# Optimization experiments

Measured on AMD Instinct MI355X. Metric: run time of the kernel, lower is better.

The kernel has to match this reference:

```python
import jax, jax.numpy as jnp
import numpy as np

HIDDEN = 1024
NUM_HEADS = 16
HEAD_SIZE = HIDDEN // NUM_HEADS


def setup_inputs() -> dict:
    key = jax.random.key(0)
    ks = jax.random.split(key, 5)
    B, S = 2, 2048
    x = jax.random.normal(ks[0], (B, S, HIDDEN), dtype=jnp.float32)
    # nn.Linear(hidden, 3*hidden): weight stored (in, out) for x @ W
    scale_qkv = 1.0 / np.sqrt(HIDDEN)
    w_qkv = jax.random.uniform(ks[1], (HIDDEN, 3 * HIDDEN), minval=-scale_qkv, maxval=scale_qkv, dtype=jnp.float32)
    b_qkv = jax.random.uniform(ks[2], (3 * HIDDEN,), minval=-scale_qkv, maxval=scale_qkv, dtype=jnp.float32)
    w_o = jax.random.uniform(ks[3], (HIDDEN, HIDDEN), minval=-scale_qkv, maxval=scale_qkv, dtype=jnp.float32)
    b_o = jax.random.uniform(ks[4], (HIDDEN,), minval=-scale_qkv, maxval=scale_qkv, dtype=jnp.float32)
    return {"x": x, "w_qkv": w_qkv, "b_qkv": b_qkv, "w_o": w_o, "b_o": b_o}


def reference(x, w_qkv, b_qkv, w_o, b_o):
    B, S, H = x.shape
    qkv = x @ w_qkv + b_qkv  # (B, S, 3H)
    q, k, v = jnp.split(qkv, 3, axis=-1)
    # (B, S, H) -> (B, nheads, S, head_size)
    def heads(t):
        return t.reshape(B, S, NUM_HEADS, HEAD_SIZE).transpose(0, 2, 1, 3)
    q, k, v = heads(q), heads(k), heads(v)
    scores = jnp.einsum('bhqd,bhkd->bhqk', q, k) / np.sqrt(HEAD_SIZE).astype(np.float32)
    causal = jnp.tril(jnp.ones((S, S), dtype=bool))  # k <= q
    scores = jnp.where(causal, scores, -jnp.inf)
    probs = jax.nn.softmax(scores, axis=-1)
    out = jnp.einsum('bhqk,bhkd->bqhd', probs, v).reshape(B, S, H)
    return out @ w_o + b_o
```

## Files before the change

kernel.cpp:

```cpp
#include <hip/hip_runtime.h>
#include <stdint.h>


typedef __bf16 bf16;
typedef __attribute__((ext_vector_type(8))) __bf16 bf16x8;
typedef __attribute__((ext_vector_type(4))) __bf16 bf16x4;
typedef __attribute__((ext_vector_type(4))) float floatx4;
typedef __attribute__((ext_vector_type(16))) float floatx16;
typedef __attribute__((ext_vector_type(4))) unsigned int uint4v;
typedef __attribute__((ext_vector_type(2))) unsigned int uint2v;

#define SCL 0.18033688011112042f

__device__ __forceinline__ floatx4 mfma_bf16(bf16x8 a, bf16x8 b, floatx4 c) {
  return __builtin_amdgcn_mfma_f32_16x16x32_bf16(a, b, c, 0, 0, 0);
}

__device__ __forceinline__ floatx16 mfma32(bf16x8 a, bf16x8 b, floatx16 c) {
  return __builtin_amdgcn_mfma_f32_32x32x16_bf16(a, b, c, 0, 0, 0);
}

__device__ __forceinline__ void cp_g2l_16(const bf16* g, bf16* l) {
  __builtin_amdgcn_global_load_lds(
      (const __attribute__((address_space(1))) void*)g,
      (__attribute__((address_space(3))) void*)l, 16, 0, 0);
}

__device__ __forceinline__ floatx16 zero16() {
  floatx16 z;
#pragma unroll
  for (int i = 0; i < 16; ++i) z[i] = 0.f;
  return z;
}

__device__ __forceinline__ uint32_t pack2(float lo, float hi2) {
  union { bf16 h[2]; uint32_t u; } x;
  x.h[0] = (bf16)lo; x.h[1] = (bf16)hi2;
  return x.u;
}

__device__ __forceinline__ uint2v permswap(uint32_t a, uint32_t b) {
  return __builtin_amdgcn_permlane32_swap(a, b, false, false);
}

__device__ __forceinline__ bf16x8 mk_pf(uint32_t w0, uint32_t w1, uint32_t w2,
                                        uint32_t w3) {
  union { uint4v u; bf16x8 v; } c;
  c.u = (uint4v){w0, w1, w2, w3};
  return c.v;
}

__global__ __launch_bounds__(256) void prep_kernel(
    const float* __restrict__ x, bf16* __restrict__ xb,
    const float* __restrict__ w_qkv, bf16* __restrict__ wqkvt,
    const float* __restrict__ w_o, bf16* __restrict__ wot) {
  const int b = blockIdx.x;
  const int tid = threadIdx.x;
  if (b < 4096) {
    const int i = (b * 256 + tid) * 4;
    floatx4 v = *(const floatx4*)(x + i);
    bf16x4 o;
    o[0] = (bf16)v[0]; o[1] = (bf16)v[1]; o[2] = (bf16)v[2]; o[3] = (bf16)v[3];
    *(bf16x4*)(xb + i) = o;
    return;
  }
  __shared__ float tile[32][33];
  const float* W; bf16* Wt; int K, N, n0, k0;
  if (b < 7168) {
    const int bb = b - 4096;
    W = w_qkv; Wt = wqkvt; K = 1024; N = 3072;
    n0 = (bb % 96) * 32; k0 = (bb / 96) * 32;
  } else {
    const int bb = b - 7168;
    W = w_o; Wt = wot; K = 1024; N = 1024;
    n0 = (bb & 31) * 32; k0 = (bb >> 5) * 32;
  }
  const int tx = tid & 31, ty = tid >> 5;
  for (int i = 0; i < 4; ++i)
    tile[ty + 8 * i][tx] = W[(size_t)(k0 + ty + 8 * i) * N + n0 + tx];
  __syncthreads();
  for (int i = 0; i < 4; ++i)
    Wt[(size_t)(n0 + ty + 8 * i) * K + k0 + tx] = (bf16)tile[tx][ty + 8 * i];
}

template <int MODE, int MI>
__global__ __launch_bounds__(256, 3) void gemm_bt_kernel(
    const bf16* __restrict__ A, const bf16* __restrict__ Bt,
    const float* __restrict__ bias, float* __restrict__ outF,
    bf16* __restrict__ qb, bf16* __restrict__ kb, bf16* __restrict__ vtb,
    int N, int K) {
  constexpr int BM = MI * 32;
  __shared__ bf16 As[BM * 32];
  __shared__ bf16 Bs[128 * 32];
  const int tid = threadIdx.x;
  const int w = tid >> 6, lane = tid & 63;
  const int l16 = lane & 15, quad = lane >> 4;
  const int m0 = blockIdx.y * BM, n0 = blockIdx.x * 128;
  const int wm = (w & 1) * (BM / 2), wn = (w >> 1) * 64;

  const int arow = w * (BM / 4) + (lane >> 2);
  const int acol = (lane & 3) * 8;
  const bf16* Ag = A + (size_t)(m0 + arow) * K + acol;
  bf16* Al = As + arow * 32 + acol;
  const int brow = w * 32 + (lane >> 2);
  const bf16* Bg = Bt + (size_t)(n0 + brow) * K + acol;
  bf16* Bl = Bs + brow * 32 + acol;

  floatx4 acc[MI][4];
#pragma unroll
  for (int i = 0; i < MI; ++i)
#pragma unroll
    for (int j = 0; j < 4; ++j) acc[i][j] = (floatx4){0.f, 0.f, 0.f, 0.f};

  for (int k0 = 0; k0 < K; k0 += 32) {
    __syncthreads();
    cp_g2l_16(Ag + k0, Al);
    if (MI == 4) cp_g2l_16(Ag + (size_t)16 * K + k0, Al + 16 * 32);
    cp_g2l_16(Bg + k0, Bl);
    cp_g2l_16(Bg + (size_t)16 * K + k0, Bl + 16 * 32);
    __syncthreads();
    bf16x8 af[MI], bfr[4];
#pragma unroll
    for (int i = 0; i < MI; ++i)
      af[i] = *(const bf16x8*)(&As[(wm + i * 16 + l16) * 32 + quad * 8]);
#pragma unroll
    for (int j = 0; j < 4; ++j)
      bfr[j] = *(const bf16x8*)(&Bs[(wn + j * 16 + l16) * 32 + quad * 8]);
#pragma unroll
    for (int i = 0; i < MI; ++i)
#pragma unroll
      for (int j = 0; j < 4; ++j)
        acc[i][j] = mfma_bf16(af[i], bfr[j], acc[i][j]);
  }

#pragma unroll
  for (int i = 0; i < MI; ++i)
#pragma unroll
    for (int j = 0; j < 4; ++j) {
      const int nn = n0 + wn + j * 16 + l16;
      const float bv = bias[nn];
      const int mbase = m0 + wm + i * 16 + quad * 4;
      if (MODE == 1) {
#pragma unroll
        for (int r = 0; r < 4; ++r)
          outF[(size_t)(mbase + r) * N + nn] = acc[i][j][r] + bv;
      } else {
        const int which = nn >> 10;
        const int rem = nn & 1023;
        const int h = rem >> 6, d = rem & 63;
        const int b = mbase >> 11, s = mbase & 2047;
        const size_t bh = (size_t)(b * 16 + h);
        if (which == 2) {
          bf16x4 pk;
#pragma unroll
          for (int r = 0; r < 4; ++r) pk[r] = (bf16)(acc[i][j][r] + bv);
          *(bf16x4*)(vtb + (bh * 64 + d) * 2048 + s) = pk;
        } else if (which == 0) {
#pragma unroll
          for (int r = 0; r < 4; ++r)
            qb[(bh * 2048 + s + r) * 64 + d] = (bf16)((acc[i][j][r] + bv) * SCL);
        } else {
#pragma unroll
          for (int r = 0; r < 4; ++r)
            kb[(bh * 2048 + s + r) * 64 + d] = (bf16)(acc[i][j][r] + bv);
        }
      }
    }
}

__global__ __launch_bounds__(256, 4) void attn_kernel(
    const bf16* __restrict__ Qb, const bf16* __restrict__ Kb,
    const bf16* __restrict__ Vtb, bf16* __restrict__ attnb) {
  __shared__ bf16 Ks[2][4096];
  __shared__ bf16 Vs[2][4096];
  const int bid = blockIdx.x;
  const int c = bid & 255, qq = bid >> 8;
  const int bh = c & 31;
  const int kk = c >> 5;
  const int g = (qq == 0) ? kk : (qq == 1) ? 31 - kk
              : (qq == 2) ? 8 + kk : 23 - kk;
  const int tid = threadIdx.x;
  const int w = tid >> 6, lane = tid & 63;
  const int l31 = lane & 31, hi = lane >> 5;
  const int strip = w >> 1, ms = w & 1;
  const int q0s = g * 64 + strip * 32;
  const int b = bh >> 4, h = bh & 15;
  const int nt = g + 1;

  const bf16* Qh = Qb + (size_t)bh * 2048 * 64;
  const bf16* Kh = Kb + (size_t)bh * 2048 * 64;
  const bf16* Vh = Vtb + (size_t)bh * 64 * 2048;

  const int c0 = tid, c1 = tid + 256;
  const int kof0 = (c0 >> 3) * 64 + ((((c0 & 7) - (c0 >> 3)) & 7) * 8);
  const int kof1 = (c1 >> 3) * 64 + ((((c1 & 7) - (c1 >> 3)) & 7) * 8);
  const int vof0 = (c0 >> 3) * 2048 + ((((c0 & 7) - (c0 >> 3)) & 7) * 8);
  const int vof1 = (c1 >> 3) * 2048 + ((((c1 & 7) - (c1 >> 3)) & 7) * 8);

  bf16x8 qf[4];
  {
    const bf16* Qr = Qh + (size_t)(q0s + l31) * 64 + hi * 8;
#pragma unroll
    for (int kd = 0; kd < 4; ++kd) qf[kd] = *(const bf16x8*)(Qr + kd * 16);
  }
  bf16x8 ones;
#pragma unroll
  for (int j = 0; j < 8; ++j) ones[j] = (bf16)1.0f;

  floatx16 O0 = zero16(), O1 = zero16(), Ol = zero16();

  cp_g2l_16(Kh + kof0, &Ks[0][c0 * 8]);
  cp_g2l_16(Kh + kof1, &Ks[0][c1 * 8]);
  cp_g2l_16(Vh + vof0, &Vs[0][c0 * 8]);
  cp_g2l_16(Vh + vof1, &Vs[0][c1 * 8]);

  int cur = 0;
  for (int t = 0; t < nt; ++t, cur ^= 1) {
    __syncthreads();
    if (t + 1 < nt) {
      const int nb = cur ^ 1;
      cp_g2l_16(Kh + (size_t)(t + 1) * 4096 + kof0, &Ks[nb][c0 * 8]);
      cp_g2l_16(Kh + (size_t)(t + 1) * 4096 + kof1, &Ks[nb][c1 * 8]);
      cp_g2l_16(Vh + (size_t)(t + 1) * 64 + vof0, &Vs[nb][c0 * 8]);
      cp_g2l_16(Vh + (size_t)(t + 1) * 64 + vof1, &Vs[nb][c1 * 8]);
    }
    const bool diag = (t == g);
    if (diag && strip == 0 && ms == 1) continue;
    const bf16* KsC = Ks[cur];
    const bf16* VsC = Vs[cur];

    floatx16 sf = zero16();
    const int row = ms * 32 + l31;
#pragma unroll
    for (int kd = 0; kd < 4; ++kd) {
      bf16x8 kf = *(const bf16x8*)(
          &KsC[row * 64 + (((kd * 2 + hi) + row) & 7) * 8]);
      sf = mfma32(kf, qf[kd], sf);
    }

    const int ksA = ms * 2, ksB = ms * 2 + 1;
    const int r0 = l31, r1 = 32 + l31;
    bf16x8 va0 = *(const bf16x8*)(&VsC[r0 * 64 + (((ksA * 2 + hi) + r0) & 7) * 8]);
    bf16x8 va1 = *(const bf16x8*)(&VsC[r1 * 64 + (((ksA * 2 + hi) + r1) & 7) * 8]);
    bf16x8 vb0 = *(const bf16x8*)(&VsC[r0 * 64 + (((ksB * 2 + hi) + r0) & 7) * 8]);
    bf16x8 vb1 = *(const bf16x8*)(&VsC[r1 * 64 + (((ksB * 2 + hi) + r1) & 7) * 8]);

    float e[16];
#pragma unroll
    for (int r = 0; r < 16; ++r) {
      float s = sf[r];
      if (diag) {
        const int kc = t * 64 + ms * 32 + (r & 3) + 8 * (r >> 2) + 4 * hi;
        s = (kc <= q0s + l31) ? s : -1e30f;
      }
      e[r] = __builtin_amdgcn_exp2f(s);
    }

    uint32_t W[8];
#pragma unroll
    for (int i = 0; i < 8; ++i) W[i] = pack2(e[2 * i], e[2 * i + 1]);
    uint2v s0 = permswap(W[0], W[2]);
    uint2v s1 = permswap(W[1], W[3]);
    bf16x8 pa = mk_pf(s0.x, s1.x, s0.y, s1.y);
    uint2v s2 = permswap(W[4], W[6]);
    uint2v s3 = permswap(W[5], W[7]);
    bf16x8 pb = mk_pf(s2.x, s3.x, s2.y, s3.y);

    O0 = mfma32(pa, va0, O0);
    O1 = mfma32(pa, va1, O1);
    Ol = mfma32(pa, ones, Ol);
    O0 = mfma32(pb, vb0, O0);
    O1 = mfma32(pb, vb1, O1);
    Ol = mfma32(pb, ones, Ol);
  }

  __syncthreads();
  float* fO = (float*)(&Ks[0][0]);
  float* fL = (float*)(&Vs[0][0]);
  if (ms == 1) {
#pragma unroll
    for (int r = 0; r < 16; ++r) {
      const int ql = (r & 3) + 8 * (r >> 2) + 4 * hi;
      fO[strip * 2048 + ql * 64 + l31] = O0[r];
      fO[strip * 2048 + ql * 64 + 32 + l31] = O1[r];
      if (l31 == 0) fL[strip * 32 + ql] = Ol[r];
    }
  }
  __syncthreads();
  if (ms == 0) {
#pragma unroll
    for (int r = 0; r < 16; ++r) {
      const int ql = (r & 3) + 8 * (r >> 2) + 4 * hi;
      O0[r] += fO[strip * 2048 + ql * 64 + l31];
      O1[r] += fO[strip * 2048 + ql * 64 + 32 + l31];
      Ol[r] += fL[strip * 32 + ql];
    }
#pragma unroll
    for (int r = 0; r < 16; ++r) {
      const int q = q0s + (r & 3) + 8 * (r >> 2) + 4 * hi;
      const float inv = 1.f / Ol[r];
      bf16* dst = attnb + ((size_t)(b * 2048 + q)) * 1024 + h * 64;
      dst[l31] = (bf16)(O0[r] * inv);
      dst[32 + l31] = (bf16)(O1[r] * inv);
    }
  }
}

extern "C" void kernel_launch(void* const* d_in, const int* in_sizes, int n_in,
                              void* d_out, int out_size, void* d_ws, size_t ws_size,
                              hipStream_t stream) {
  const float* x     = (const float*)d_in[0];
  const float* w_qkv = (const float*)d_in[1];
  const float* b_qkv = (const float*)d_in[2];
  const float* w_o   = (const float*)d_in[3];
  const float* b_o   = (const float*)d_in[4];
  float* out = (float*)d_out;

  char* ws = (char*)d_ws;
  bf16* xb    = (bf16*)ws; ws += (size_t)4096 * 1024 * 2;
  bf16* wqkvt = (bf16*)ws; ws += (size_t)3072 * 1024 * 2;
  bf16* wot   = (bf16*)ws; ws += (size_t)1024 * 1024 * 2;
  bf16* qb    = (bf16*)ws; ws += (size_t)32 * 2048 * 64 * 2;
  bf16* kb    = (bf16*)ws; ws += (size_t)32 * 2048 * 64 * 2;
  bf16* vtb   = (bf16*)ws; ws += (size_t)32 * 2048 * 64 * 2;
  bf16* attnb = (bf16*)ws; ws += (size_t)4096 * 1024 * 2;

  prep_kernel<<<8192, 256, 0, stream>>>(x, xb, w_qkv, wqkvt, w_o, wot);
  gemm_bt_kernel<0, 4><<<dim3(24, 32), 256, 0, stream>>>(
      xb, wqkvt, b_qkv, nullptr, qb, kb, vtb, 3072, 1024);
  attn_kernel<<<1024, 256, 0, stream>>>(qb, kb, vtb, attnb);
  gemm_bt_kernel<1, 2><<<dim3(8, 64), 256, 0, stream>>>(
      attnb, wot, b_o, out, nullptr, nullptr, nullptr, 1024, 1024);
}
```

Measured before the change: 176.4 us.

## Software-pipeline attention loop: overlap next QK^T with previous PV MFMAs

Restructures the attention inner loop so that the P·V MFMAs for tile t-1 are issued alongside the QK^T MFMAs for tile t, with exp/pack for tile t done afterward. V shared-memory staging grows from double to triple buffering so the previous tile's V stays valid while the next tile is prefetched, and a drain step after the loop handles the last tile. The goal is to hide exp and pack latency behind matrix work. In exchange it uses more LDS per block (which may reduce occupancy) and holds the packed probabilities in registers across iterations.

```diff
diff --git a/kernel.cpp b/kernel.cpp
--- a/kernel.cpp
+++ b/kernel.cpp
@@ -172,7 +172,7 @@
     const bf16* __restrict__ Qb, const bf16* __restrict__ Kb,
     const bf16* __restrict__ Vtb, bf16* __restrict__ attnb) {
   __shared__ bf16 Ks[2][4096];
-  __shared__ bf16 Vs[2][4096];
+  __shared__ bf16 Vs[3][4096];
   const int bid = blockIdx.x;
   const int c = bid & 255, qq = bid >> 8;
   const int bh = c & 31;
@@ -214,64 +214,95 @@
   cp_g2l_16(Vh + vof0, &Vs[0][c0 * 8]);
   cp_g2l_16(Vh + vof1, &Vs[0][c1 * 8]);
 
-  int cur = 0;
-  for (int t = 0; t < nt; ++t, cur ^= 1) {
+  const int ksA = ms * 2, ksB = ms * 2 + 1;
+  const int r0 = l31, r1 = 32 + l31;
+  bf16x8 paS, pbS;
+  int havePrev = 0;
+  int kcur = 0;
+  int vStage = 1;
+
+  for (int t = 0; t < nt; ++t) {
+    const int vPrev = (vStage == 2) ? 0 : vStage + 1;
     __syncthreads();
     if (t + 1 < nt) {
-      const int nb = cur ^ 1;
-      cp_g2l_16(Kh + (size_t)(t + 1) * 4096 + kof0, &Ks[nb][c0 * 8]);
-      cp_g2l_16(Kh + (size_t)(t + 1) * 4096 + kof1, &Ks[nb][c1 * 8]);
-      cp_g2l_16(Vh + (size_t)(t + 1) * 64 + vof0, &Vs[nb][c0 * 8]);
-      cp_g2l_16(Vh + (size_t)(t + 1) * 64 + vof1, &Vs[nb][c1 * 8]);
+      cp_g2l_16(Kh + (size_t)(t + 1) * 4096 + kof0, &Ks[kcur ^ 1][c0 * 8]);
+      cp_g2l_16(Kh + (size_t)(t + 1) * 4096 + kof1, &Ks[kcur ^ 1][c1 * 8]);
+      cp_g2l_16(Vh + (size_t)(t + 1) * 64 + vof0, &Vs[vStage][c0 * 8]);
+      cp_g2l_16(Vh + (size_t)(t + 1) * 64 + vof1, &Vs[vStage][c1 * 8]);
     }
     const bool diag = (t == g);
-    if (diag && strip == 0 && ms == 1) continue;
-    const bf16* KsC = Ks[cur];
-    const bf16* VsC = Vs[cur];
-
-    floatx16 sf = zero16();
-    const int row = ms * 32 + l31;
-#pragma unroll
-    for (int kd = 0; kd < 4; ++kd) {
-      bf16x8 kf = *(const bf16x8*)(
-          &KsC[row * 64 + (((kd * 2 + hi) + row) & 7) * 8]);
-      sf = mfma32(kf, qf[kd], sf);
-    }
-
-    const int ksA = ms * 2, ksB = ms * 2 + 1;
-    const int r0 = l31, r1 = 32 + l31;
-    bf16x8 va0 = *(const bf16x8*)(&VsC[r0 * 64 + (((ksA * 2 + hi) + r0) & 7) * 8]);
-    bf16x8 va1 = *(const bf16x8*)(&VsC[r1 * 64 + (((ksA * 2 + hi) + r1) & 7) * 8]);
-    bf16x8 vb0 = *(const bf16x8*)(&VsC[r0 * 64 + (((ksB * 2 + hi) + r0) & 7) * 8]);
-    bf16x8 vb1 = *(const bf16x8*)(&VsC[r1 * 64 + (((ksB * 2 + hi) + r1) & 7) * 8]);
-
-    float e[16];
-#pragma unroll
-    for (int r = 0; r < 16; ++r) {
-      float s = sf[r];
-      if (diag) {
-        const int kc = t * 64 + ms * 32 + (r & 3) + 8 * (r >> 2) + 4 * hi;
-        s = (kc <= q0s + l31) ? s : -1e30f;
+    const bool skip = diag && strip == 0 && ms == 1;
+
+    bf16x8 va0, va1, vb0, vb1;
+    if (havePrev) {
+      const bf16* VsP = &Vs[vPrev][0];
+      va0 = *(const bf16x8*)(&VsP[r0 * 64 + (((ksA * 2 + hi) + r0) & 7) * 8]);
+      va1 = *(const bf16x8*)(&VsP[r1 * 64 + (((ksA * 2 + hi) + r1) & 7) * 8]);
+      vb0 = *(const bf16x8*)(&VsP[r0 * 64 + (((ksB * 2 + hi) + r0) & 7) * 8]);
+      vb1 = *(const bf16x8*)(&VsP[r1 * 64 + (((ksB * 2 + hi) + r1) & 7) * 8]);
+    }
+
+    floatx16 sf;
+    if (!skip) {
+      sf = zero16();
+      const bf16* KsC = &Ks[kcur][0];
+      const int row = ms * 32 + l31;
+#pragma unroll
+      for (int kd = 0; kd < 4; ++kd) {
+        bf16x8 kf = *(const bf16x8*)(
+            &KsC[row * 64 + (((kd * 2 + hi) + row) & 7) * 8]);
+        sf = mfma32(kf, qf[kd], sf);
       }
-      e[r] = __builtin_amdgcn_exp2f(s);
-    }
-
-    uint32_t W[8];
-#pragma unroll
-    for (int i = 0; i < 8; ++i) W[i] = pack2(e[2 * i], e[2 * i + 1]);
-    uint2v s0 = permswap(W[0], W[2]);
-    uint2v s1 = permswap(W[1], W[3]);
-    bf16x8 pa = mk_pf(s0.x, s1.x, s0.y, s1.y);
-    uint2v s2 = permswap(W[4], W[6]);
-    uint2v s3 = permswap(W[5], W[7]);
-    bf16x8 pb = mk_pf(s2.x, s3.x, s2.y, s3.y);
-
-    O0 = mfma32(pa, va0, O0);
-    O1 = mfma32(pa, va1, O1);
-    Ol = mfma32(pa, ones, Ol);
-    O0 = mfma32(pb, vb0, O0);
-    O1 = mfma32(pb, vb1, O1);
-    Ol = mfma32(pb, ones, Ol);
+    }
+
+    if (havePrev) {
+      O0 = mfma32(paS, va0, O0);
+      O1 = mfma32(paS, va1, O1);
+      Ol = mfma32(paS, ones, Ol);
+      O0 = mfma32(pbS, vb0, O0);
+      O1 = mfma32(pbS, vb1, O1);
+      Ol = mfma32(pbS, ones, Ol);
+    }
+
+    if (!skip) {
+      float e[16];
+#pragma unroll
+      for (int r = 0; r < 16; ++r) {
+        float s = sf[r];
+        if (diag) {
+          const int kc = t * 64 + ms * 32 + (r & 3) + 8 * (r >> 2) + 4 * hi;
+          s = (kc <= q0s + l31) ? s : -1e30f;
+        }
+        e[r] = __builtin_amdgcn_exp2f(s);
+      }
+      uint32_t W[8];
+#pragma unroll
+      for (int i = 0; i < 8; ++i) W[i] = pack2(e[2 * i], e[2 * i + 1]);
+      uint2v s0 = permswap(W[0], W[2]);
+      uint2v s1 = permswap(W[1], W[3]);
+      paS = mk_pf(s0.x, s1.x, s0.y, s1.y);
+      uint2v s2 = permswap(W[4], W[6]);
+      uint2v s3 = permswap(W[5], W[7]);
+      pbS = mk_pf(s2.x, s3.x, s2.y, s3.y);
+    }
+    havePrev = !skip;
+    kcur ^= 1;
+    vStage = vPrev;
+  }
+
+  if (havePrev) {
+    const int vPrev = (vStage == 2) ? 0 : vStage + 1;
+    const bf16* VsP = &Vs[vPrev][0];
+    bf16x8 va0 = *(const bf16x8*)(&VsP[r0 * 64 + (((ksA * 2 + hi) + r0) & 7) * 8]);
+    bf16x8 va1 = *(const bf16x8*)(&VsP[r1 * 64 + (((ksA * 2 + hi) + r1) & 7) * 8]);
+    bf16x8 vb0 = *(const bf16x8*)(&VsP[r0 * 64 + (((ksB * 2 + hi) + r0) & 7) * 8]);
+    bf16x8 vb1 = *(const bf16x8*)(&VsP[r1 * 64 + (((ksB * 2 + hi) + r1) & 7) * 8]);
+    O0 = mfma32(paS, va0, O0);
+    O1 = mfma32(paS, va1, O1);
+    Ol = mfma32(paS, ones, Ol);
+    O0 = mfma32(pbS, vb0, O0);
+    O1 = mfma32(pbS, vb1, O1);
+    Ol = mfma32(pbS, ones, Ol);
   }
 
   __syncthreads();
```

Result: slower. 181.0 us (+2.6%).

## Load attention K/V straight from global memory and use 32-row query blocks

Applied to the files above, without the earlier changes.

The attention kernel stops staging K and V tiles in shared memory with double-buffered async copies. Each wave now loads its K and V fragments directly from global memory into registers. Blocks shrink to two waves covering one 32-row query strip, with twice as many blocks and a new diagonal-balanced strip ordering. This removes per-tile barriers and LDS traffic and raises occupancy. The cost is that K/V are no longer shared across strips within a block, so more global and L2 reads are issued.

```diff
diff --git a/kernel.cpp b/kernel.cpp
--- a/kernel.cpp
+++ b/kernel.cpp
@@ -168,35 +168,28 @@
     }
 }
 
-__global__ __launch_bounds__(256, 4) void attn_kernel(
+__global__ __launch_bounds__(128, 4) void attn_kernel(
     const bf16* __restrict__ Qb, const bf16* __restrict__ Kb,
     const bf16* __restrict__ Vtb, bf16* __restrict__ attnb) {
-  __shared__ bf16 Ks[2][4096];
-  __shared__ bf16 Vs[2][4096];
+  __shared__ float fO[2048];
+  __shared__ float fL[32];
   const int bid = blockIdx.x;
   const int c = bid & 255, qq = bid >> 8;
   const int bh = c & 31;
   const int kk = c >> 5;
-  const int g = (qq == 0) ? kk : (qq == 1) ? 31 - kk
-              : (qq == 2) ? 8 + kk : 23 - kk;
+  const int st = (qq < 4) ? (kk * 4 + qq) : (63 - (kk * 4 + qq - 4));
   const int tid = threadIdx.x;
-  const int w = tid >> 6, lane = tid & 63;
+  const int ms = tid >> 6, lane = tid & 63;
   const int l31 = lane & 31, hi = lane >> 5;
-  const int strip = w >> 1, ms = w & 1;
-  const int q0s = g * 64 + strip * 32;
+  const int q0s = st * 32;
   const int b = bh >> 4, h = bh & 15;
-  const int nt = g + 1;
+  const int g = st >> 1;
+  const int myNt = ((st & 1) == 0 && ms == 1) ? g : g + 1;
 
   const bf16* Qh = Qb + (size_t)bh * 2048 * 64;
   const bf16* Kh = Kb + (size_t)bh * 2048 * 64;
   const bf16* Vh = Vtb + (size_t)bh * 64 * 2048;
 
-  const int c0 = tid, c1 = tid + 256;
-  const int kof0 = (c0 >> 3) * 64 + ((((c0 & 7) - (c0 >> 3)) & 7) * 8);
-  const int kof1 = (c1 >> 3) * 64 + ((((c1 & 7) - (c1 >> 3)) & 7) * 8);
-  const int vof0 = (c0 >> 3) * 2048 + ((((c0 & 7) - (c0 >> 3)) & 7) * 8);
-  const int vof1 = (c1 >> 3) * 2048 + ((((c1 & 7) - (c1 >> 3)) & 7) * 8);
-
   bf16x8 qf[4];
   {
     const bf16* Qr = Qh + (size_t)(q0s + l31) * 64 + hi * 8;
@@ -209,41 +202,29 @@
 
   floatx16 O0 = zero16(), O1 = zero16(), Ol = zero16();
 
-  cp_g2l_16(Kh + kof0, &Ks[0][c0 * 8]);
-  cp_g2l_16(Kh + kof1, &Ks[0][c1 * 8]);
-  cp_g2l_16(Vh + vof0, &Vs[0][c0 * 8]);
-  cp_g2l_16(Vh + vof1, &Vs[0][c1 * 8]);
-
-  int cur = 0;
-  for (int t = 0; t < nt; ++t, cur ^= 1) {
-    __syncthreads();
-    if (t + 1 < nt) {
-      const int nb = cur ^ 1;
-      cp_g2l_16(Kh + (size_t)(t + 1) * 4096 + kof0, &Ks[nb][c0 * 8]);
-      cp_g2l_16(Kh + (size_t)(t + 1) * 4096 + kof1, &Ks[nb][c1 * 8]);
-      cp_g2l_16(Vh + (size_t)(t + 1) * 64 + vof0, &Vs[nb][c0 * 8]);
-      cp_g2l_16(Vh + (size_t)(t + 1) * 64 + vof1, &Vs[nb][c1 * 8]);
-    }
+  const bf16* Kr = Kh + (size_t)(ms * 32 + l31) * 64 + hi * 8;
+  const bf16* Vr0 = Vh + (size_t)l31 * 2048 + ms * 32 + hi * 8;
+  const bf16* Vr1 = Vr0 + (size_t)32 * 2048;
+
+  for (int t = 0; t < myNt; ++t) {
     const bool diag = (t == g);
-    if (diag && strip == 0 && ms == 1) continue;
-    const bf16* KsC = Ks[cur];
-    const bf16* VsC = Vs[cur];
+
+    const bf16* Kt = Kr + (size_t)t * 4096;
+    bf16x8 kf0 = *(const bf16x8*)(Kt);
+    bf16x8 kf1 = *(const bf16x8*)(Kt + 16);
+    bf16x8 kf2 = *(const bf16x8*)(Kt + 32);
+    bf16x8 kf3 = *(const bf16x8*)(Kt + 48);
+
+    bf16x8 va0 = *(const bf16x8*)(Vr0 + t * 64);
+    bf16x8 va1 = *(const bf16x8*)(Vr1 + t * 64);
+    bf16x8 vb0 = *(const bf16x8*)(Vr0 + t * 64 + 16);
+    bf16x8 vb1 = *(const bf16x8*)(Vr1 + t * 64 + 16);
 
     floatx16 sf = zero16();
-    const int row = ms * 32 + l31;
-#pragma unroll
-    for (int kd = 0; kd < 4; ++kd) {
-      bf16x8 kf = *(const bf16x8*)(
-          &KsC[row * 64 + (((kd * 2 + hi) + row) & 7) * 8]);
-      sf = mfma32(kf, qf[kd], sf);
-    }
-
-    const int ksA = ms * 2, ksB = ms * 2 + 1;
-    const int r0 = l31, r1 = 32 + l31;
-    bf16x8 va0 = *(const bf16x8*)(&VsC[r0 * 64 + (((ksA * 2 + hi) + r0) & 7) * 8]);
-    bf16x8 va1 = *(const bf16x8*)(&VsC[r1 * 64 + (((ksA * 2 + hi) + r1) & 7) * 8]);
-    bf16x8 vb0 = *(const bf16x8*)(&VsC[r0 * 64 + (((ksB * 2 + hi) + r0) & 7) * 8]);
-    bf16x8 vb1 = *(const bf16x8*)(&VsC[r1 * 64 + (((ksB * 2 + hi) + r1) & 7) * 8]);
+    sf = mfma32(kf0, qf[0], sf);
+    sf = mfma32(kf1, qf[1], sf);
+    sf = mfma32(kf2, qf[2], sf);
+    sf = mfma32(kf3, qf[3], sf);
 
     float e[16];
 #pragma unroll
@@ -275,15 +256,13 @@
   }
 
   __syncthreads();
-  float* fO = (float*)(&Ks[0][0]);
-  float* fL = (float*)(&Vs[0][0]);
   if (ms == 1) {
 #pragma unroll
     for (int r = 0; r < 16; ++r) {
       const int ql = (r & 3) + 8 * (r >> 2) + 4 * hi;
-      fO[strip * 2048 + ql * 64 + l31] = O0[r];
-      fO[strip * 2048 + ql * 64 + 32 + l31] = O1[r];
-      if (l31 == 0) fL[strip * 32 + ql] = Ol[r];
+      fO[ql * 64 + l31] = O0[r];
+      fO[ql * 64 + 32 + l31] = O1[r];
+      if (l31 == 0) fL[ql] = Ol[r];
     }
   }
   __syncthreads();
@@ -291,17 +270,12 @@
 #pragma unroll
     for (int r = 0; r < 16; ++r) {
       const int ql = (r & 3) + 8 * (r >> 2) + 4 * hi;
-      O0[r] += fO[strip * 2048 + ql * 64 + l31];
-      O1[r] += fO[strip * 2048 + ql * 64 + 32 + l31];
-      Ol[r] += fL[strip * 32 + ql];
-    }
-#pragma unroll
-    for (int r = 0; r < 16; ++r) {
-      const int q = q0s + (r & 3) + 8 * (r >> 2) + 4 * hi;
-      const float inv = 1.f / Ol[r];
-      bf16* dst = attnb + ((size_t)(b * 2048 + q)) * 1024 + h * 64;
-      dst[l31] = (bf16)(O0[r] * inv);
-      dst[32 + l31] = (bf16)(O1[r] * inv);
+      const float o0 = O0[r] + fO[ql * 64 + l31];
+      const float o1 = O1[r] + fO[ql * 64 + 32 + l31];
+      const float inv = 1.f / (Ol[r] + fL[ql]);
+      bf16* dst = attnb + ((size_t)(b * 2048 + q0s + ql)) * 1024 + h * 64;
+      dst[l31] = (bf16)(o0 * inv);
+      dst[32 + l31] = (bf16)(o1 * inv);
     }
   }
 }
@@ -328,7 +302,7 @@
   prep_kernel<<<8192, 256, 0, stream>>>(x, xb, w_qkv, wqkvt, w_o, wot);
   gemm_bt_kernel<0, 4><<<dim3(24, 32), 256, 0, stream>>>(
       xb, wqkvt, b_qkv, nullptr, qb, kb, vtb, 3072, 1024);
-  attn_kernel<<<1024, 256, 0, stream>>>(qb, kb, vtb, attnb);
+  attn_kernel<<<2048, 128, 0, stream>>>(qb, kb, vtb, attnb);
   gemm_bt_kernel<1, 2><<<dim3(8, 64), 256, 0, stream>>>(
       attnb, wot, b_o, out, nullptr, nullptr, nullptr, 1024, 1024);
 }
```

After: 202.2 us. 14.6% more time.

## Triple-buffer K tiles with split vmcnt waits and MFMA priority hints

Applied to the files above, without the earlier changes.

Reworks the attention kernel's load pipeline so K tiles are prefetched two iterations ahead in a three-slot LDS ring, while V stays double-buffered one iteration ahead. Explicit vmcnt waits let the V load still be in flight during the QK^T MFMAs and the exp, instead of blocking on everything at the loop-top barrier. It also raises wave priority around the MFMA blocks and merges the epilogue loops. The cost is extra LDS, which may reduce occupancy, and hand-written waitcnt and barrier logic that is fragile. Every iteration now issues loads, including some redundant dummy loads at the tail.

```diff
diff --git a/kernel.cpp b/kernel.cpp
--- a/kernel.cpp
+++ b/kernel.cpp
@@ -171,7 +171,7 @@
 __global__ __launch_bounds__(256, 4) void attn_kernel(
     const bf16* __restrict__ Qb, const bf16* __restrict__ Kb,
     const bf16* __restrict__ Vtb, bf16* __restrict__ attnb) {
-  __shared__ bf16 Ks[2][4096];
+  __shared__ bf16 Ks[3][4096];
   __shared__ bf16 Vs[2][4096];
   const int bid = blockIdx.x;
   const int c = bid & 255, qq = bid >> 8;
@@ -209,69 +209,90 @@
 
   floatx16 O0 = zero16(), O1 = zero16(), Ol = zero16();
 
-  cp_g2l_16(Kh + kof0, &Ks[0][c0 * 8]);
-  cp_g2l_16(Kh + kof1, &Ks[0][c1 * 8]);
-  cp_g2l_16(Vh + vof0, &Vs[0][c0 * 8]);
-  cp_g2l_16(Vh + vof1, &Vs[0][c1 * 8]);
-
-  int cur = 0;
-  for (int t = 0; t < nt; ++t, cur ^= 1) {
-    __syncthreads();
-    if (t + 1 < nt) {
-      const int nb = cur ^ 1;
-      cp_g2l_16(Kh + (size_t)(t + 1) * 4096 + kof0, &Ks[nb][c0 * 8]);
-      cp_g2l_16(Kh + (size_t)(t + 1) * 4096 + kof1, &Ks[nb][c1 * 8]);
-      cp_g2l_16(Vh + (size_t)(t + 1) * 64 + vof0, &Vs[nb][c0 * 8]);
-      cp_g2l_16(Vh + (size_t)(t + 1) * 64 + vof1, &Vs[nb][c1 * 8]);
-    }
+  {
+    const int k1 = (1 < nt) ? 1 : 0;
+    cp_g2l_16(Kh + kof0, &Ks[0][c0 * 8]);
+    cp_g2l_16(Kh + kof1, &Ks[0][c1 * 8]);
+    cp_g2l_16(Kh + (size_t)k1 * 4096 + kof0, &Ks[1][c0 * 8]);
+    cp_g2l_16(Kh + (size_t)k1 * 4096 + kof1, &Ks[1][c1 * 8]);
+    cp_g2l_16(Vh + vof0, &Vs[0][c0 * 8]);
+    cp_g2l_16(Vh + vof1, &Vs[0][c1 * 8]);
+    asm volatile("s_waitcnt vmcnt(4)" ::: "memory");
+    __builtin_amdgcn_sched_barrier(0);
+  }
+
+  int kr = 0;
+  for (int t = 0; t < nt; ++t) {
+    __builtin_amdgcn_s_barrier();
+    __builtin_amdgcn_sched_barrier(0);
+
+    {
+      const int tk = (t + 2 < nt) ? t + 2 : 0;
+      const int tv = (t + 1 < nt) ? t + 1 : 0;
+      const int kst = (kr >= 1) ? kr - 1 : 2;
+      cp_g2l_16(Kh + (size_t)tk * 4096 + kof0, &Ks[kst][c0 * 8]);
+      cp_g2l_16(Kh + (size_t)tk * 4096 + kof1, &Ks[kst][c1 * 8]);
+      cp_g2l_16(Vh + (size_t)tv * 64 + vof0, &Vs[(t + 1) & 1][c0 * 8]);
+      cp_g2l_16(Vh + (size_t)tv * 64 + vof1, &Vs[(t + 1) & 1][c1 * 8]);
+    }
+
     const bool diag = (t == g);
-    if (diag && strip == 0 && ms == 1) continue;
-    const bf16* KsC = Ks[cur];
-    const bf16* VsC = Vs[cur];
-
-    floatx16 sf = zero16();
-    const int row = ms * 32 + l31;
-#pragma unroll
-    for (int kd = 0; kd < 4; ++kd) {
-      bf16x8 kf = *(const bf16x8*)(
-          &KsC[row * 64 + (((kd * 2 + hi) + row) & 7) * 8]);
-      sf = mfma32(kf, qf[kd], sf);
-    }
-
-    const int ksA = ms * 2, ksB = ms * 2 + 1;
-    const int r0 = l31, r1 = 32 + l31;
-    bf16x8 va0 = *(const bf16x8*)(&VsC[r0 * 64 + (((ksA * 2 + hi) + r0) & 7) * 8]);
-    bf16x8 va1 = *(const bf16x8*)(&VsC[r1 * 64 + (((ksA * 2 + hi) + r1) & 7) * 8]);
-    bf16x8 vb0 = *(const bf16x8*)(&VsC[r0 * 64 + (((ksB * 2 + hi) + r0) & 7) * 8]);
-    bf16x8 vb1 = *(const bf16x8*)(&VsC[r1 * 64 + (((ksB * 2 + hi) + r1) & 7) * 8]);
-
-    float e[16];
-#pragma unroll
-    for (int r = 0; r < 16; ++r) {
-      float s = sf[r];
-      if (diag) {
-        const int kc = t * 64 + ms * 32 + (r & 3) + 8 * (r >> 2) + 4 * hi;
-        s = (kc <= q0s + l31) ? s : -1e30f;
+    if (!(diag && strip == 0 && ms == 1)) {
+      const bf16* KsC = &Ks[kr][0];
+
+      floatx16 sf = zero16();
+      const int row = ms * 32 + l31;
+      __builtin_amdgcn_s_setprio(1);
+#pragma unroll
+      for (int kd = 0; kd < 4; ++kd) {
+        bf16x8 kf = *(const bf16x8*)(
+            &KsC[row * 64 + (((kd * 2 + hi) + row) & 7) * 8]);
+        sf = mfma32(kf, qf[kd], sf);
       }
-      e[r] = __builtin_amdgcn_exp2f(s);
-    }
-
-    uint32_t W[8];
-#pragma unroll
-    for (int i = 0; i < 8; ++i) W[i] = pack2(e[2 * i], e[2 * i + 1]);
-    uint2v s0 = permswap(W[0], W[2]);
-    uint2v s1 = permswap(W[1], W[3]);
-    bf16x8 pa = mk_pf(s0.x, s1.x, s0.y, s1.y);
-    uint2v s2 = permswap(W[4], W[6]);
-    uint2v s3 = permswap(W[5], W[7]);
-    bf16x8 pb = mk_pf(s2.x, s3.x, s2.y, s3.y);
-
-    O0 = mfma32(pa, va0, O0);
-    O1 = mfma32(pa, va1, O1);
-    Ol = mfma32(pa, ones, Ol);
-    O0 = mfma32(pb, vb0, O0);
-    O1 = mfma32(pb, vb1, O1);
-    Ol = mfma32(pb, ones, Ol);
+      __builtin_amdgcn_s_setprio(0);
+
+      float e[16];
+#pragma unroll
+      for (int r = 0; r < 16; ++r) {
+        float s = sf[r];
+        if (diag) {
+          const int kc = t * 64 + ms * 32 + (r & 3) + 8 * (r >> 2) + 4 * hi;
+          s = (kc <= q0s + l31) ? s : -1e30f;
+        }
+        e[r] = __builtin_amdgcn_exp2f(s);
+      }
+
+      uint32_t W[8];
+#pragma unroll
+      for (int i = 0; i < 8; ++i) W[i] = pack2(e[2 * i], e[2 * i + 1]);
+      uint2v s0 = permswap(W[0], W[2]);
+      uint2v s1 = permswap(W[1], W[3]);
+      bf16x8 pa = mk_pf(s0.x, s1.x, s0.y, s1.y);
+      uint2v s2 = permswap(W[4], W[6]);
+      uint2v s3 = permswap(W[5], W[7]);
+      bf16x8 pb = mk_pf(s2.x, s3.x, s2.y, s3.y);
+
+      asm volatile("s_waitcnt vmcnt(4)" ::: "memory");
+      __builtin_amdgcn_sched_barrier(0);
+
+      const bf16* VsC = &Vs[t & 1][0];
+      const int ksA = ms * 2, ksB = ms * 2 + 1;
+      const int r0 = l31, r1 = 32 + l31;
+      bf16x8 va0 = *(const bf16x8*)(&VsC[r0 * 64 + (((ksA * 2 + hi) + r0) & 7) * 8]);
+      bf16x8 va1 = *(const bf16x8*)(&VsC[r1 * 64 + (((ksA * 2 + hi) + r1) & 7) * 8]);
+      bf16x8 vb0 = *(const bf16x8*)(&VsC[r0 * 64 + (((ksB * 2 + hi) + r0) & 7) * 8]);
+      bf16x8 vb1 = *(const bf16x8*)(&VsC[r1 * 64 + (((ksB * 2 + hi) + r1) & 7) * 8]);
+
+      __builtin_amdgcn_s_setprio(1);
+      O0 = mfma32(pa, va0, O0);
+      O1 = mfma32(pa, va1, O1);
+      Ol = mfma32(pa, ones, Ol);
+      O0 = mfma32(pb, vb0, O0);
+      O1 = mfma32(pb, vb1, O1);
+      Ol = mfma32(pb, ones, Ol);
+      __builtin_amdgcn_s_setprio(0);
+    }
+    kr = (kr == 2) ? 0 : kr + 1;
   }
 
   __syncthreads();
@@ -291,17 +312,12 @@
 #pragma unroll
     for (int r = 0; r < 16; ++r) {
       const int ql = (r & 3) + 8 * (r >> 2) + 4 * hi;
-      O0[r] += fO[strip * 2048 + ql * 64 + l31];
-      O1[r] += fO[strip * 2048 + ql * 64 + 32 + l31];
-      Ol[r] += fL[strip * 32 + ql];
-    }
-#pragma unroll
-    for (int r = 0; r < 16; ++r) {
-      const int q = q0s + (r & 3) + 8 * (r >> 2) + 4 * hi;
-      const float inv = 1.f / Ol[r];
-      bf16* dst = attnb + ((size_t)(b * 2048 + q)) * 1024 + h * 64;
-      dst[l31] = (bf16)(O0[r] * inv);
-      dst[32 + l31] = (bf16)(O1[r] * inv);
+      const float o0 = O0[r] + fO[strip * 2048 + ql * 64 + l31];
+      const float o1 = O1[r] + fO[strip * 2048 + ql * 64 + 32 + l31];
+      const float inv = 1.f / (Ol[r] + fL[strip * 32 + ql]);
+      bf16* dst = attnb + ((size_t)(b * 2048 + q0s + ql)) * 1024 + h * 64;
+      dst[l31] = (bf16)(o0 * inv);
+      dst[32 + l31] = (bf16)(o1 * inv);
     }
   }
 }
```

Result: faster. 170.9 us (-3.2%).
